# Performance work log

Measured on AMD Instinct MI355X. Metric: run time of the kernel, lower is better.

The kernel has to match this reference:

```python
import jax, jax.numpy as jnp
import numpy as np

D_MODEL = 1024
NUM_HEADS = 16
D_FF = 4096
EPS = 1e-5


def _linear(x, w, b):
    # torch nn.Linear: y = x @ W^T + b, W is [out, in]
    return jnp.einsum('bld,od->blo', x, w) + b


def _layer_norm(x, g, b):
    mu = jnp.mean(x, axis=-1, keepdims=True)
    var = jnp.mean(jnp.square(x - mu), axis=-1, keepdims=True)
    return (x - mu) / jnp.sqrt(var + EPS) * g + b


def _mha(q, k, v, wq, bq, wk, bk, wv, bv, wo, bo, mask, num_heads):
    B, Lq, D = q.shape
    hd = D // num_heads
    Q = _linear(q, wq, bq).reshape(B, Lq, num_heads, hd).transpose(0, 2, 1, 3)
    K = _linear(k, wk, bk).reshape(B, -1, num_heads, hd).transpose(0, 2, 1, 3)
    V = _linear(v, wv, bv).reshape(B, -1, num_heads, hd).transpose(0, 2, 1, 3)
    scale = jnp.sqrt(jnp.asarray(hd, dtype=q.dtype))
    energy = jnp.einsum('bhqd,bhkd->bhqk', Q, K) / scale  # [B,H,Lq,Lk]
    energy = jnp.where(mask, energy, jnp.asarray(-1e10, dtype=q.dtype))
    attn = jax.nn.softmax(energy, axis=-1)
    x = jnp.einsum('bhqk,bhkd->bhqd', attn, V)
    x = x.transpose(0, 2, 1, 3).reshape(B, Lq, D)
    return _linear(x, wo, bo), attn


def setup_inputs() -> dict:
    key = jax.random.key(0)
    ks = iter(jax.random.split(key, 40))
    B, T, S, D, F = 4, 1024, 1024, D_MODEL, D_FF
    inp = {
        'tgt': jax.random.normal(next(ks), (B, T, D), dtype=jnp.float32),
        'enc_src': jax.random.normal(next(ks), (B, S, D), dtype=jnp.float32),
        'tgt_mask': jnp.tril(jnp.ones((1, 1, T, T), dtype=bool)),
        'src_mask': jnp.ones((1, 1, 1, S), dtype=bool),
    }
    def lin(kk, o, i):
        return jax.random.normal(kk, (o, i), dtype=jnp.float32) * 0.02
    for pfx in ('sa', 'ca'):  # self-attn and cross-attn params
        for nm in ('q', 'k', 'v', 'o'):
            inp[f'{pfx}_w{nm}'] = lin(next(ks), D, D)
            inp[f'{pfx}_b{nm}'] = jnp.zeros((D,), dtype=jnp.float32)
    inp['ff_w1'] = lin(next(ks), F, D)
    inp['ff_b1'] = jnp.zeros((F,), dtype=jnp.float32)
    inp['ff_w2'] = lin(next(ks), D, F)
    inp['ff_b2'] = jnp.zeros((D,), dtype=jnp.float32)
    for i in (1, 2, 3):
        inp[f'ln{i}_g'] = jnp.ones((D,), dtype=jnp.float32)
        inp[f'ln{i}_b'] = jnp.zeros((D,), dtype=jnp.float32)
    return inp


def reference(tgt, enc_src, tgt_mask, src_mask,
              sa_wq, sa_bq, sa_wk, sa_bk, sa_wv, sa_bv, sa_wo, sa_bo,
              ca_wq, ca_bq, ca_wk, ca_bk, ca_wv, ca_bv, ca_wo, ca_bo,
              ff_w1, ff_b1, ff_w2, ff_b2,
              ln1_g, ln1_b, ln2_g, ln2_b, ln3_g, ln3_b):
    # dropout in eval mode (identity)
    _t, _ = _mha(tgt, tgt, tgt, sa_wq, sa_bq, sa_wk, sa_bk, sa_wv, sa_bv,
                 sa_wo, sa_bo, tgt_mask, NUM_HEADS)
    tgt = _layer_norm(tgt + _t, ln1_g, ln1_b)
    _t, attention = _mha(tgt, enc_src, enc_src, ca_wq, ca_bq, ca_wk, ca_bk,
                         ca_wv, ca_bv, ca_wo, ca_bo, src_mask, NUM_HEADS)
    tgt = _layer_norm(tgt + _t, ln2_g, ln2_b)
    _t = _linear(jax.nn.relu(_linear(tgt, ff_w1, ff_b1)), ff_w2, ff_b2)
    tgt = _layer_norm(tgt + _t, ln3_g, ln3_b)
    return tgt, attention
```

## Files before the change

### kernel.cpp

```cpp
#include <hip/hip_runtime.h>
#include <hip/hip_bf16.h>

#define BBATCH 4
#define TT 1024
#define SS 1024
#define DD 1024
#define HH 16
#define HD 64
#define FFD 4096
#define MM (BBATCH*TT)

using f32x4  = __attribute__((ext_vector_type(4))) float;
using s16x8  = __attribute__((ext_vector_type(8))) short;
using bf16x8 = __attribute__((ext_vector_type(8))) __bf16;

__device__ __forceinline__ unsigned short f2b(float f) {
  union { float f; unsigned int u; } x{f};
  unsigned int r = x.u + 0x7FFFu + ((x.u >> 16) & 1u);
  return (unsigned short)(r >> 16);
}

__device__ __forceinline__ float b2f(unsigned short u) {
  union { unsigned int i; float f; } x; x.i = (unsigned int)u << 16; return x.f;
}

__device__ __forceinline__ void gload16(const void* g, void* l) {
  __builtin_amdgcn_global_load_lds(
      (const __attribute__((address_space(1))) void*)g,
      (__attribute__((address_space(3))) void*)l, 16, 0, 0);
}

__device__ __forceinline__ f32x4 mfma_bf16(s16x8 a, s16x8 b, f32x4 c) {
  return __builtin_amdgcn_mfma_f32_16x16x32_bf16(
      __builtin_bit_cast(bf16x8, a), __builtin_bit_cast(bf16x8, b), c, 0, 0, 0);
}

template <int JT, int NSUB>
__device__ __forceinline__ void gemm_core(
    const unsigned short* __restrict__ Ab, int lda,
    const unsigned short* __restrict__ Bb, int ldb,
    int K, unsigned short* As, unsigned short* Bs, f32x4 (&acc)[4][JT])
{
  const int tid = threadIdx.x, wave = tid >> 6, lane = tid & 63;
  const int r0 = tid >> 2, c0 = (tid & 3) * 8;
  const int wrow = (wave >> 1) * 64, wcol = (wave & 1) * 16 * JT;
  const int q = lane >> 4, rl = lane & 15;
  const s16x8* Av = (const s16x8*)As;
  const s16x8* Bv = (const s16x8*)Bs;

  for (int k0 = 0; k0 < K; k0 += 32 * NSUB) {
#pragma unroll
    for (int s = 0; s < NSUB; s++) {
      int kk = k0 + s * 32;
      gload16(Ab + (size_t)r0 * lda + kk + c0, As + s * 4096 + wave * 512);
      gload16(Ab + (size_t)(r0 + 64) * lda + kk + c0, As + s * 4096 + wave * 512 + 2048);
      gload16(Bb + (size_t)r0 * ldb + kk + c0, Bs + s * (JT * 1024) + wave * 512);
      if (JT == 4)
        gload16(Bb + (size_t)(r0 + 64) * ldb + kk + c0, Bs + s * (JT * 1024) + wave * 512 + 2048);
    }
    __syncthreads();
#pragma unroll
    for (int s = 0; s < NSUB; s++) {
      s16x8 af[4], bfr[JT];
#pragma unroll
      for (int t = 0; t < 4; t++) af[t] = Av[s * 512 + (wrow + t * 16 + rl) * 4 + q];
#pragma unroll
      for (int t = 0; t < JT; t++) bfr[t] = Bv[s * (JT * 128) + (wcol + t * 16 + rl) * 4 + q];
#pragma unroll
      for (int i = 0; i < 4; i++)
#pragma unroll
        for (int j = 0; j < JT; j++)
          acc[i][j] = mfma_bf16(af[i], bfr[j], acc[i][j]);
    }
    __syncthreads();
  }
}

template <int EPI, int JT, int NSUB>
__global__ __launch_bounds__(256) void gemm_bt(
    const unsigned short* __restrict__ A, int lda,
    const unsigned short* __restrict__ B, int ldb,
    const float* __restrict__ bias, const float* __restrict__ res,
    float* __restrict__ Cf, unsigned short* __restrict__ Cb, int ldc, int K)
{
  __shared__ __align__(16) unsigned short As[NSUB * 128 * 32];
  __shared__ __align__(16) unsigned short Bs[NSUB * JT * 1024];
  const int bm = blockIdx.y, bn = blockIdx.x;
  const int lane = threadIdx.x & 63, wave = threadIdx.x >> 6;
  const int wrow = (wave >> 1) * 64, wcol = (wave & 1) * 16 * JT;
  const int q = lane >> 4, rl = lane & 15;

  f32x4 acc[4][JT];
  f32x4 z = {0.f, 0.f, 0.f, 0.f};
#pragma unroll
  for (int i = 0; i < 4; i++)
#pragma unroll
    for (int j = 0; j < JT; j++) acc[i][j] = z;

  gemm_core<JT, NSUB>(A + (size_t)bm * 128 * lda, lda,
                      B + (size_t)bn * (32 * JT) * ldb, ldb, K, As, Bs, acc);

#pragma unroll
  for (int i = 0; i < 4; i++) {
    int gm0 = bm * 128 + wrow + i * 16 + q * 4;
#pragma unroll
    for (int j = 0; j < JT; j++) {
      int gn = bn * (32 * JT) + wcol + j * 16 + rl;
      float bv = bias[gn];
#pragma unroll
      for (int r = 0; r < 4; r++) {
        size_t off = (size_t)(gm0 + r) * ldc + gn;
        float v = acc[i][j][r];
        if constexpr (EPI == 0) Cb[off] = f2b(v + bv);
        else if constexpr (EPI == 2) Cf[off] = v + bv + res[off];
        else Cb[off] = f2b(fmaxf(v + bv, 0.f));
      }
    }
  }
}

__device__ __forceinline__ void sblock_qk(
    const unsigned short* Qs, const unsigned short* Ks,
    int wrow, int wcol, int q, int rl, f32x4 (&acc)[4][4])
{
  const s16x8* Qv = (const s16x8*)Qs;
  const s16x8* Kv = (const s16x8*)Ks;
  f32x4 z = {0.f, 0.f, 0.f, 0.f};
#pragma unroll
  for (int i = 0; i < 4; i++)
#pragma unroll
    for (int j = 0; j < 4; j++) acc[i][j] = z;
#pragma unroll
  for (int kq = 0; kq < 2; kq++) {
    s16x8 af[4], bf[4];
#pragma unroll
    for (int t = 0; t < 4; t++) af[t] = Qv[kq * 512 + (wrow + t * 16 + rl) * 4 + q];
#pragma unroll
    for (int t = 0; t < 4; t++) bf[t] = Kv[kq * 512 + (wcol + t * 16 + rl) * 4 + q];
#pragma unroll
    for (int i = 0; i < 4; i++)
#pragma unroll
      for (int j = 0; j < 4; j++)
        acc[i][j] = mfma_bf16(af[i], bf[j], acc[i][j]);
  }
}

__device__ __forceinline__ void store_ps_swz(
    unsigned short* Ps, const f32x4 (&acc)[4][4], int wrow, int wcol, int q, int rl)
{
#pragma unroll
  for (int i = 0; i < 4; i++)
#pragma unroll
    for (int j = 0; j < 4; j++) {
      int col = wcol + j * 16 + rl;
      int ks = col >> 5, cc = col & 31;
#pragma unroll
      for (int r = 0; r < 4; r++) {
        int row = wrow + i * 16 + q * 4 + r;
        int unit = (row * 4 + (cc >> 3)) ^ ((row >> 1) & 3);
        Ps[ks * 4096 + unit * 8 + (cc & 7)] = f2b(acc[i][j][r]);
      }
    }
}

__device__ __forceinline__ void pv_swz(
    const unsigned short* Ps, const unsigned short* Vs,
    int wrow, int wc2, int q, int rl, f32x4 (&oacc)[4][2])
{
  const s16x8* Pv = (const s16x8*)Ps;
  const s16x8* Vv = (const s16x8*)Vs;
#pragma unroll
  for (int ks = 0; ks < 4; ks++) {
    s16x8 af[4], bf[2];
#pragma unroll
    for (int t = 0; t < 4; t++) {
      int row = wrow + t * 16 + rl;
      af[t] = Pv[ks * 512 + ((row * 4 + q) ^ ((row >> 1) & 3))];
    }
#pragma unroll
    for (int t = 0; t < 2; t++) bf[t] = Vv[ks * 256 + (wc2 + t * 16 + rl) * 4 + q];
#pragma unroll
    for (int i = 0; i < 4; i++)
#pragma unroll
      for (int jt = 0; jt < 2; jt++)
        oacc[i][jt] = mfma_bf16(af[i], bf[jt], oacc[i][jt]);
  }
}

__global__ __launch_bounds__(256, 2) void flash_sa(
    const unsigned short* __restrict__ Qg, int ldq,
    const unsigned short* __restrict__ Kg, int ldk,
    const unsigned short* __restrict__ Vt,
    unsigned short* __restrict__ Og)
{
  __shared__ __align__(16) unsigned short Qs[2 * 128 * 32];
  __shared__ __align__(16) unsigned short Ks[2 * 128 * 32];
  __shared__ __align__(16) unsigned short Vs[4 * 64 * 32];
  __shared__ __align__(16) unsigned short Ps[4 * 128 * 32];

  const int tid = threadIdx.x, wave = tid >> 6, lane = tid & 63;
  const int q = lane >> 4, rl = lane & 15;
  const int bh = blockIdx.y, b = bh >> 4, h = bh & 15;
  const int bm = (bh & 32) ? (7 - blockIdx.x) : blockIdx.x;
  const int wrow = (wave >> 1) * 64, wcol = (wave & 1) * 64;
  const int wc2 = (wave & 1) * 32;
  const int r0 = tid >> 2, c0 = (tid & 3) * 8;

  const unsigned short* Qbase = Qg + ((size_t)b * TT + bm * 128) * ldq + h * HD;
  const unsigned short* Kbase = Kg + (size_t)b * SS * ldk + h * HD;
  const unsigned short* Vbase = Vt + ((size_t)bh << 16);

#pragma unroll
  for (int kq = 0; kq < 2; kq++) {
    gload16(Qbase + (size_t)r0 * ldq + kq * 32 + c0, Qs + kq * 4096 + wave * 512);
    gload16(Qbase + (size_t)(r0 + 64) * ldq + kq * 32 + c0, Qs + kq * 4096 + wave * 512 + 2048);
  }
  const int nch = bm + 1;

  float l_run[4][4];
  f32x4 oacc[4][2];
  f32x4 z = {0.f, 0.f, 0.f, 0.f};
#pragma unroll
  for (int i = 0; i < 4; i++) {
    oacc[i][0] = z; oacc[i][1] = z;
#pragma unroll
    for (int r = 0; r < 4; r++) l_run[i][r] = 0.f;
  }

  for (int c = 0; c < nch; c++) {
    const unsigned short* src = Kbase + (size_t)c * 128 * ldk;
#pragma unroll
    for (int kq = 0; kq < 2; kq++) {
      gload16(src + (size_t)r0 * ldk + kq * 32 + c0, Ks + kq * 4096 + wave * 512);
      gload16(src + (size_t)(r0 + 64) * ldk + kq * 32 + c0, Ks + kq * 4096 + wave * 512 + 2048);
    }
#pragma unroll
    for (int ks = 0; ks < 4; ks++)
      gload16(Vbase + (size_t)r0 * SS + c * 128 + ks * 32 + c0, Vs + ks * 2048 + wave * 512);
    __syncthreads();

    f32x4 acc[4][4];
    sblock_qk(Qs, Ks, wrow, wcol, q, rl, acc);
#pragma unroll
    for (int i = 0; i < 4; i++)
#pragma unroll
      for (int r = 0; r < 4; r++) {
#pragma unroll
        for (int j = 0; j < 4; j++) {
          float v = acc[i][j][r] * 0.125f;
          bool msk = (c == bm) && (wcol + j * 16 + rl) > (wrow + i * 16 + q * 4 + r);
          acc[i][j][r] = msk ? 0.f : __expf(v);
        }
        float s = acc[i][0][r] + acc[i][1][r] + acc[i][2][r] + acc[i][3][r];
#pragma unroll
        for (int off = 1; off < 16; off <<= 1) s += __shfl_xor(s, off);
        l_run[i][r] += s;
      }
    store_ps_swz(Ps, acc, wrow, wcol, q, rl);
    __syncthreads();
    pv_swz(Ps, Vs, wrow, wc2, q, rl, oacc);
    __syncthreads();
  }

  float* red = (float*)Ps;
  if (rl == 0) {
#pragma unroll
    for (int i = 0; i < 4; i++)
#pragma unroll
      for (int r = 0; r < 4; r++)
        red[(wave & 1) * 128 + wrow + i * 16 + q * 4 + r] = l_run[i][r];
  }
  __syncthreads();

#pragma unroll
  for (int i = 0; i < 4; i++) {
#pragma unroll
    for (int r = 0; r < 4; r++) {
      int row = wrow + i * 16 + q * 4 + r;
      float inv = 1.0f / (red[row] + red[128 + row]);
      int grow = bm * 128 + row;
#pragma unroll
      for (int jt = 0; jt < 2; jt++) {
        int col = h * HD + wc2 + jt * 16 + rl;
        Og[((size_t)b * TT + grow) * DD + col] = f2b(oacc[i][jt][r] * inv);
      }
    }
  }
}

__global__ __launch_bounds__(256, 2) void flash_ca(
    const unsigned short* __restrict__ Qg, int ldq,
    const unsigned short* __restrict__ Kg, int ldk,
    const unsigned short* __restrict__ Vt,
    float* __restrict__ Pout,
    unsigned short* __restrict__ Og)
{
  __shared__ __align__(16) unsigned short Qs[2 * 128 * 32];
  __shared__ __align__(16) unsigned short Ks[2 * 128 * 32];
  __shared__ __align__(16) unsigned short Vs[4 * 64 * 32];
  __shared__ __align__(16) unsigned short Ps[4 * 128 * 32];

  const int tid = threadIdx.x, wave = tid >> 6, lane = tid & 63;
  const int q = lane >> 4, rl = lane & 15;
  const int bm = blockIdx.x, bh = blockIdx.y, b = bh >> 4, h = bh & 15;
  const int wrow = (wave >> 1) * 64, wcol = (wave & 1) * 64;
  const int wc2 = (wave & 1) * 32;
  const int r0 = tid >> 2, c0 = (tid & 3) * 8;

  const unsigned short* Qbase = Qg + ((size_t)b * TT + bm * 128) * ldq + h * HD;
  const unsigned short* Kbase = Kg + (size_t)b * SS * ldk + h * HD;
  const unsigned short* Vbase = Vt + ((size_t)bh << 16);

#pragma unroll
  for (int kq = 0; kq < 2; kq++) {
    gload16(Qbase + (size_t)r0 * ldq + kq * 32 + c0, Qs + kq * 4096 + wave * 512);
    gload16(Qbase + (size_t)(r0 + 64) * ldq + kq * 32 + c0, Qs + kq * 4096 + wave * 512 + 2048);
  }

  float l_run[4][4];
#pragma unroll
  for (int i = 0; i < 4; i++)
#pragma unroll
    for (int r = 0; r < 4; r++) l_run[i][r] = 0.f;

  for (int c = 0; c < 8; c++) {
    const unsigned short* src = Kbase + (size_t)c * 128 * ldk;
#pragma unroll
    for (int kq = 0; kq < 2; kq++) {
      gload16(src + (size_t)r0 * ldk + kq * 32 + c0, Ks + kq * 4096 + wave * 512);
      gload16(src + (size_t)(r0 + 64) * ldk + kq * 32 + c0, Ks + kq * 4096 + wave * 512 + 2048);
    }
    __syncthreads();
    f32x4 acc[4][4];
    sblock_qk(Qs, Ks, wrow, wcol, q, rl, acc);
#pragma unroll
    for (int i = 0; i < 4; i++)
#pragma unroll
      for (int r = 0; r < 4; r++) {
        float s = __expf(acc[i][0][r] * 0.125f) + __expf(acc[i][1][r] * 0.125f) +
                  __expf(acc[i][2][r] * 0.125f) + __expf(acc[i][3][r] * 0.125f);
#pragma unroll
        for (int off = 1; off < 16; off <<= 1) s += __shfl_xor(s, off);
        l_run[i][r] += s;
      }
    __syncthreads();
  }
  float* red = (float*)Ps;
  if (rl == 0) {
#pragma unroll
    for (int i = 0; i < 4; i++)
#pragma unroll
      for (int r = 0; r < 4; r++)
        red[(wave & 1) * 128 + wrow + i * 16 + q * 4 + r] = l_run[i][r];
  }
  __syncthreads();
  float invl[4][4];
#pragma unroll
  for (int i = 0; i < 4; i++)
#pragma unroll
    for (int r = 0; r < 4; r++) {
      int row = wrow + i * 16 + q * 4 + r;
      invl[i][r] = 1.0f / (red[row] + red[128 + row]);
    }

  f32x4 oacc[4][2];
  f32x4 z = {0.f, 0.f, 0.f, 0.f};
#pragma unroll
  for (int i = 0; i < 4; i++) { oacc[i][0] = z; oacc[i][1] = z; }

  for (int c = 0; c < 8; c++) {
    const unsigned short* src = Kbase + (size_t)c * 128 * ldk;
#pragma unroll
    for (int kq = 0; kq < 2; kq++) {
      gload16(src + (size_t)r0 * ldk + kq * 32 + c0, Ks + kq * 4096 + wave * 512);
      gload16(src + (size_t)(r0 + 64) * ldk + kq * 32 + c0, Ks + kq * 4096 + wave * 512 + 2048);
    }
#pragma unroll
    for (int ks = 0; ks < 4; ks++)
      gload16(Vbase + (size_t)r0 * SS + c * 128 + ks * 32 + c0, Vs + ks * 2048 + wave * 512);
    __syncthreads();
    f32x4 acc[4][4];
    sblock_qk(Qs, Ks, wrow, wcol, q, rl, acc);
#pragma unroll
    for (int i = 0; i < 4; i++)
#pragma unroll
      for (int j = 0; j < 4; j++)
#pragma unroll
        for (int r = 0; r < 4; r++)
          acc[i][j][r] = __expf(acc[i][j][r] * 0.125f) * invl[i][r];
    store_ps_swz(Ps, acc, wrow, wcol, q, rl);
    __syncthreads();
#pragma unroll
    for (int it = 0; it < 8; it++) {
      int idx = it * 256 + tid;
      int ks = idx >> 9, rw = (idx >> 2) & 127, u = idx & 3;
      s16x8 pv = ((const s16x8*)Ps)[ks * 512 + ((rw * 4 + u) ^ ((rw >> 1) & 3))];
      float4 lo = make_float4(b2f((unsigned short)pv[0]), b2f((unsigned short)pv[1]),
                              b2f((unsigned short)pv[2]), b2f((unsigned short)pv[3]));
      float4 hi = make_float4(b2f((unsigned short)pv[4]), b2f((unsigned short)pv[5]),
                              b2f((unsigned short)pv[6]), b2f((unsigned short)pv[7]));
      float* dst = Pout + ((size_t)bh << 20) + ((size_t)(bm * 128 + rw) << 10) +
                   c * 128 + ks * 32 + u * 8;
      ((float4*)dst)[0] = lo;
      ((float4*)dst)[1] = hi;
    }
    pv_swz(Ps, Vs, wrow, wc2, q, rl, oacc);
    __syncthreads();
  }

#pragma unroll
  for (int i = 0; i < 4; i++)
#pragma unroll
    for (int jt = 0; jt < 2; jt++)
#pragma unroll
      for (int r = 0; r < 4; r++) {
        int row = bm * 128 + wrow + i * 16 + q * 4 + r;
        int col = h * HD + wc2 + jt * 16 + rl;
        Og[((size_t)b * TT + row) * DD + col] = f2b(oacc[i][jt][r]);
      }
}

__global__ __launch_bounds__(256) void transpose_v(
    const unsigned short* __restrict__ V, int ldv, unsigned short* __restrict__ Vt)
{
  __shared__ unsigned short tile[64][68];
  const int bh = blockIdx.z, b = bh >> 4, h = bh & 15;
  const int s0 = blockIdx.x * 64;
  const int tid = threadIdx.x;
#pragma unroll
  for (int i = 0; i < 4; i++) {
    int idx = i * 256 + tid;
    int sl = idx >> 4, d0 = (idx & 15) * 4;
    ushort4 v = *(const ushort4*)&V[((size_t)b * SS + s0 + sl) * ldv + h * HD + d0];
    tile[sl][d0] = v.x; tile[sl][d0 + 1] = v.y; tile[sl][d0 + 2] = v.z; tile[sl][d0 + 3] = v.w;
  }
  __syncthreads();
#pragma unroll
  for (int i = 0; i < 4; i++) {
    int idx = i * 256 + tid;
    int d = idx >> 4, s4 = (idx & 15) * 4;
    ushort4 o = make_ushort4(tile[s4][d], tile[s4 + 1][d], tile[s4 + 2][d], tile[s4 + 3][d]);
    *(ushort4*)&Vt[((size_t)bh * HD + d) * SS + s0 + s4] = o;
  }
}

__global__ __launch_bounds__(256) void ln_k(
    const float* __restrict__ src, const float* __restrict__ g,
    const float* __restrict__ b, float* __restrict__ dstf,
    unsigned short* __restrict__ dstb)
{
  __shared__ float sh[10];
  const size_t row = blockIdx.x;
  const int tid = threadIdx.x;
  float4 v = ((const float4*)(src + (row << 10)))[tid];
  float s = v.x + v.y + v.z + v.w;
  float ss = v.x * v.x + v.y * v.y + v.z * v.z + v.w * v.w;
  for (int o = 32; o; o >>= 1) { s += __shfl_down(s, o); ss += __shfl_down(ss, o); }
  if ((tid & 63) == 0) { sh[tid >> 6] = s; sh[4 + (tid >> 6)] = ss; }
  __syncthreads();
  if (tid == 0) {
    sh[8] = sh[0] + sh[1] + sh[2] + sh[3];
    sh[9] = sh[4] + sh[5] + sh[6] + sh[7];
  }
  __syncthreads();
  const float mean = sh[8] * (1.0f / DD);
  const float var = sh[9] * (1.0f / DD) - mean * mean;
  const float inv = rsqrtf(var + 1e-5f);
  float4 gv = ((const float4*)g)[tid];
  float4 bv = ((const float4*)b)[tid];
  float4 y;
  y.x = (v.x - mean) * inv * gv.x + bv.x;
  y.y = (v.y - mean) * inv * gv.y + bv.y;
  y.z = (v.z - mean) * inv * gv.z + bv.z;
  y.w = (v.w - mean) * inv * gv.w + bv.w;
  if (dstf) ((float4*)(dstf + (row << 10)))[tid] = y;
  if (dstb) {
    ushort4 o = make_ushort4(f2b(y.x), f2b(y.y), f2b(y.z), f2b(y.w));
    ((ushort4*)(dstb + (row << 10)))[tid] = o;
  }
}

struct CvtArgs {
  const float* src[12];
  unsigned short* dst[12];
};

__global__ __launch_bounds__(256) void cvt_all(CvtArgs a) {
  constexpr int st[13] = {0,       1048576, 2097152, 2359296, 2621440,
                          2883584, 3145728, 3407872, 3670016, 3932160,
                          4194304, 5242880, 6291456};
  int i = blockIdx.x * 256 + threadIdx.x;
  int s = 0;
#pragma unroll
  for (int k = 1; k < 12; k++) s += (i >= st[k]) ? 1 : 0;
  int j = i - st[s];
  float4 v = ((const float4*)a.src[s])[j];
  ushort4 o = make_ushort4(f2b(v.x), f2b(v.y), f2b(v.z), f2b(v.w));
  ((ushort4*)a.dst[s])[j] = o;
}

__global__ __launch_bounds__(256) void bias_pack(
    const float* __restrict__ bq, const float* __restrict__ bk, const float* __restrict__ bv,
    const float* __restrict__ bk2, const float* __restrict__ bv2,
    float* __restrict__ bqkv, float* __restrict__ bkv)
{
  int i = blockIdx.x * 256 + threadIdx.x;
  if (i < 1024) bqkv[i] = bq[i];
  else if (i < 2048) bqkv[i] = bk[i - 1024];
  else if (i < 3072) bqkv[i] = bv[i - 2048];
  else if (i < 4096) bkv[i - 3072] = bk2[i - 3072];
  else if (i < 5120) bkv[i - 3072] = bv2[i - 4096 + 1024];
}


extern "C" void kernel_launch(void* const* d_in, const int* in_sizes, int n_in,
                              void* d_out, int out_size, void* d_ws, size_t ws_size,
                              hipStream_t stream)
{
  const float* tgt = (const float*)d_in[0];
  const float* enc = (const float*)d_in[1];
  const float* sa_wq = (const float*)d_in[4];  const float* sa_bq = (const float*)d_in[5];
  const float* sa_wk = (const float*)d_in[6];  const float* sa_bk = (const float*)d_in[7];
  const float* sa_wv = (const float*)d_in[8];  const float* sa_bv = (const float*)d_in[9];
  const float* sa_wo = (const float*)d_in[10]; const float* sa_bo = (const float*)d_in[11];
  const float* ca_wq = (const float*)d_in[12]; const float* ca_bq = (const float*)d_in[13];
  const float* ca_wk = (const float*)d_in[14]; const float* ca_bk = (const float*)d_in[15];
  const float* ca_wv = (const float*)d_in[16]; const float* ca_bv = (const float*)d_in[17];
  const float* ca_wo = (const float*)d_in[18]; const float* ca_bo = (const float*)d_in[19];
  const float* ff_w1 = (const float*)d_in[20]; const float* ff_b1 = (const float*)d_in[21];
  const float* ff_w2 = (const float*)d_in[22]; const float* ff_b2 = (const float*)d_in[23];
  const float* ln1_g = (const float*)d_in[24]; const float* ln1_b = (const float*)d_in[25];
  const float* ln2_g = (const float*)d_in[26]; const float* ln2_b = (const float*)d_in[27];
  const float* ln3_g = (const float*)d_in[28]; const float* ln3_b = (const float*)d_in[29];

  float* out_tgt = (float*)d_out;
  float* out_attn = (float*)d_out + (size_t)MM * DD;

  char* w = (char*)d_ws;
  size_t off = 0;
  auto alloc = [&](size_t bytes) { void* p = w + off; off += (bytes + 255) & ~(size_t)255; return p; };
  unsigned short* Xb   = (unsigned short*)alloc((size_t)MM * DD * 2);
  unsigned short* Eb   = (unsigned short*)alloc((size_t)MM * DD * 2);
  unsigned short* Wq1  = (unsigned short*)alloc((size_t)DD * DD * 2);
  unsigned short* Wk1  = (unsigned short*)alloc((size_t)DD * DD * 2);
  unsigned short* Wv1  = (unsigned short*)alloc((size_t)DD * DD * 2);
  unsigned short* Wo1  = (unsigned short*)alloc((size_t)DD * DD * 2);
  unsigned short* Wq2  = (unsigned short*)alloc((size_t)DD * DD * 2);
  unsigned short* Wk2  = (unsigned short*)alloc((size_t)DD * DD * 2);
  unsigned short* Wv2  = (unsigned short*)alloc((size_t)DD * DD * 2);
  unsigned short* Wo2  = (unsigned short*)alloc((size_t)DD * DD * 2);
  unsigned short* Wf1  = (unsigned short*)alloc((size_t)FFD * DD * 2);
  unsigned short* Wf2  = (unsigned short*)alloc((size_t)DD * FFD * 2);
  unsigned short* QKVb = (unsigned short*)alloc((size_t)MM * 3 * DD * 2);
  unsigned short* KVb  = (unsigned short*)alloc((size_t)MM * 2 * DD * 2);
  unsigned short* Qca  = (unsigned short*)alloc((size_t)MM * DD * 2);
  unsigned short* Vt   = (unsigned short*)alloc((size_t)MM * DD * 2);
  unsigned short* Ob   = (unsigned short*)alloc((size_t)MM * DD * 2);
  float*          res1 = (float*)alloc((size_t)MM * DD * 4);
  unsigned short* t1b  = (unsigned short*)alloc((size_t)MM * DD * 2);
  float*          res2 = (float*)alloc((size_t)MM * DD * 4);
  unsigned short* t2b  = (unsigned short*)alloc((size_t)MM * DD * 2);
  unsigned short* Fb   = (unsigned short*)alloc((size_t)MM * FFD * 2);
  float*          bqkv = (float*)alloc(3072 * 4);
  float*          bkv  = (float*)alloc(2048 * 4);

  CvtArgs ca;
  ca.src[0] = tgt;   ca.dst[0] = Xb;
  ca.src[1] = enc;   ca.dst[1] = Eb;
  ca.src[2] = sa_wq; ca.dst[2] = Wq1;
  ca.src[3] = sa_wk; ca.dst[3] = Wk1;
  ca.src[4] = sa_wv; ca.dst[4] = Wv1;
  ca.src[5] = sa_wo; ca.dst[5] = Wo1;
  ca.src[6] = ca_wq; ca.dst[6] = Wq2;
  ca.src[7] = ca_wk; ca.dst[7] = Wk2;
  ca.src[8] = ca_wv; ca.dst[8] = Wv2;
  ca.src[9] = ca_wo; ca.dst[9] = Wo2;
  ca.src[10] = ff_w1; ca.dst[10] = Wf1;
  ca.src[11] = ff_w2; ca.dst[11] = Wf2;

  bias_pack<<<20, 256, 0, stream>>>(sa_bq, sa_bk, sa_bv, ca_bk, ca_bv, bqkv, bkv);
  cvt_all<<<24576, 256, 0, stream>>>(ca);

  const dim3 gQKV(24, 32);
  const dim3 gKV(16, 32);
  const dim3 gN64(16, 32);
  const dim3 gFF1(32, 32);
  const dim3 gFl(8, 64);
  const dim3 gTr(SS / 64, 1, BBATCH * HH);

  gemm_bt<0, 4, 2><<<gQKV, 256, 0, stream>>>(Xb, DD, Wq1, DD, bqkv, nullptr, nullptr, QKVb, 3 * DD, DD);
  transpose_v<<<gTr, 256, 0, stream>>>(QKVb + 2 * DD, 3 * DD, Vt);
  flash_sa<<<gFl, 256, 0, stream>>>(QKVb, 3 * DD, QKVb + DD, 3 * DD, Vt, Ob);
  gemm_bt<2, 2, 4><<<gN64, 256, 0, stream>>>(Ob, DD, Wo1, DD, sa_bo, tgt, res1, nullptr, DD, DD);
  ln_k<<<MM, 256, 0, stream>>>(res1, ln1_g, ln1_b, res1, t1b);

  gemm_bt<0, 2, 4><<<gN64, 256, 0, stream>>>(t1b, DD, Wq2, DD, ca_bq, nullptr, nullptr, Qca, DD, DD);
  gemm_bt<0, 4, 2><<<gKV, 256, 0, stream>>>(Eb, DD, Wk2, DD, bkv, nullptr, nullptr, KVb, 2 * DD, DD);
  transpose_v<<<gTr, 256, 0, stream>>>(KVb + DD, 2 * DD, Vt);
  flash_ca<<<gFl, 256, 0, stream>>>(Qca, DD, KVb, 2 * DD, Vt, out_attn, Ob);
  gemm_bt<2, 2, 4><<<gN64, 256, 0, stream>>>(Ob, DD, Wo2, DD, ca_bo, res1, res2, nullptr, DD, DD);
  ln_k<<<MM, 256, 0, stream>>>(res2, ln2_g, ln2_b, res2, t2b);

  gemm_bt<3, 4, 2><<<gFF1, 256, 0, stream>>>(t2b, DD, Wf1, DD, ff_b1, nullptr, nullptr, Fb, FFD, DD);
  gemm_bt<2, 2, 4><<<gN64, 256, 0, stream>>>(Fb, FFD, Wf2, FFD, ff_b2, res2, res1, nullptr, DD, FFD);
  ln_k<<<MM, 256, 0, stream>>>(res1, ln3_g, ln3_b, out_tgt, nullptr);
}
```

Measured before the change: 786.7 us.

## Fuse self/cross QKV projections into one GEMM with transposed-V epilogue

Merges the self-attention QKV projection and the cross-attention KV projection (which depends only on encoder input) into a single 40x32-tile GEMM launch. Tiles that produce V write their output transposed through LDS directly into per-head Vt layout, which removes both transpose_v kernels. This saves two launches, a full read and write of V, and the tail effect of two separate GEMMs. In exchange it adds a second Vt buffer and some LDS reuse after the main loop. V columns are not written to QKVb/KVb, which is fine because the flash kernels read V from Vt.

```diff
diff --git a/kernel.cpp b/kernel.cpp
--- a/kernel.cpp
+++ b/kernel.cpp
@@ -115,6 +115,87 @@
         else if constexpr (EPI == 2) Cf[off] = v + bv + res[off];
         else Cb[off] = f2b(fmaxf(v + bv, 0.f));
       }
+    }
+  }
+}
+
+__global__ __launch_bounds__(256) void gemm_qkvkv(
+    const unsigned short* __restrict__ Xb, const unsigned short* __restrict__ Eb,
+    const unsigned short* __restrict__ Wqkv1, const unsigned short* __restrict__ Wkv2,
+    const float* __restrict__ bqkv, const float* __restrict__ bkv,
+    unsigned short* __restrict__ QKVb, unsigned short* __restrict__ KVb,
+    unsigned short* __restrict__ Vt1, unsigned short* __restrict__ Vt2)
+{
+  __shared__ __align__(16) unsigned short lds[16384];
+  unsigned short* As = lds;
+  unsigned short* Bs = lds + 8192;
+  const int tid = threadIdx.x;
+  const int bm = blockIdx.y, bn = blockIdx.x;
+  const int lane = tid & 63, wave = tid >> 6;
+  const int wrow = (wave >> 1) * 64, wcol = (wave & 1) * 64;
+  const int q = lane >> 4, rl = lane & 15;
+
+  const unsigned short *A, *Bw;
+  const float* bias;
+  unsigned short *C, *Vt;
+  int ldc, vbn;
+  bool isV;
+  if (bn < 24) {
+    A = Xb; Bw = Wqkv1 + (size_t)bn * 128 * 1024; bias = bqkv + bn * 128;
+    C = QKVb + bn * 128; ldc = 3072;
+    isV = (bn >= 16); Vt = Vt1; vbn = bn - 16;
+  } else {
+    int b2 = bn - 24;
+    A = Eb; Bw = Wkv2 + (size_t)b2 * 128 * 1024; bias = bkv + b2 * 128;
+    C = KVb + b2 * 128; ldc = 2048;
+    isV = (b2 >= 8); Vt = Vt2; vbn = b2 - 8;
+  }
+
+  f32x4 acc[4][4];
+  f32x4 z = {0.f, 0.f, 0.f, 0.f};
+#pragma unroll
+  for (int i = 0; i < 4; i++)
+#pragma unroll
+    for (int j = 0; j < 4; j++) acc[i][j] = z;
+
+  gemm_core<4, 2>(A + (size_t)bm * 128 * 1024, 1024, Bw, 1024, 1024, As, Bs, acc);
+
+  if (!isV) {
+#pragma unroll
+    for (int i = 0; i < 4; i++) {
+      int lr0 = wrow + i * 16 + q * 4;
+#pragma unroll
+      for (int j = 0; j < 4; j++) {
+        int lc = wcol + j * 16 + rl;
+        float bv = bias[lc];
+#pragma unroll
+        for (int r = 0; r < 4; r++)
+          C[(size_t)(bm * 128 + lr0 + r) * ldc + lc] = f2b(acc[i][j][r] + bv);
+      }
+    }
+  } else {
+#pragma unroll
+    for (int i = 0; i < 4; i++) {
+      int lr0 = wrow + i * 16 + q * 4;
+#pragma unroll
+      for (int j = 0; j < 4; j++) {
+        int lc = wcol + j * 16 + rl;
+        float bv = bias[lc];
+        int base = lc * 128, sw = (lc & 7) << 2;
+#pragma unroll
+        for (int r = 0; r < 4; r++)
+          lds[base + ((lr0 + r) ^ sw)] = f2b(acc[i][j][r] + bv);
+      }
+    }
+    __syncthreads();
+    const int b = bm >> 3, s0 = (bm & 7) * 128;
+#pragma unroll
+    for (int it = 0; it < 16; it++) {
+      int idx = it * 256 + tid;
+      int lc = idx >> 5, qa = idx & 31;
+      ushort4 v4 = *(const ushort4*)&lds[lc * 128 + ((qa ^ (lc & 7)) << 2)];
+      int h = vbn * 2 + (lc >> 6), d = lc & 63;
+      *(ushort4*)&Vt[(((size_t)b * 16 + h) * 64 + d) * 1024 + s0 + qa * 4] = v4;
     }
   }
 }
@@ -418,30 +499,6 @@
         int col = h * HD + wc2 + jt * 16 + rl;
         Og[((size_t)b * TT + row) * DD + col] = f2b(oacc[i][jt][r]);
       }
-}
-
-__global__ __launch_bounds__(256) void transpose_v(
-    const unsigned short* __restrict__ V, int ldv, unsigned short* __restrict__ Vt)
-{
-  __shared__ unsigned short tile[64][68];
-  const int bh = blockIdx.z, b = bh >> 4, h = bh & 15;
-  const int s0 = blockIdx.x * 64;
-  const int tid = threadIdx.x;
-#pragma unroll
-  for (int i = 0; i < 4; i++) {
-    int idx = i * 256 + tid;
-    int sl = idx >> 4, d0 = (idx & 15) * 4;
-    ushort4 v = *(const ushort4*)&V[((size_t)b * SS + s0 + sl) * ldv + h * HD + d0];
-    tile[sl][d0] = v.x; tile[sl][d0 + 1] = v.y; tile[sl][d0 + 2] = v.z; tile[sl][d0 + 3] = v.w;
-  }
-  __syncthreads();
-#pragma unroll
-  for (int i = 0; i < 4; i++) {
-    int idx = i * 256 + tid;
-    int d = idx >> 4, s4 = (idx & 15) * 4;
-    ushort4 o = make_ushort4(tile[s4][d], tile[s4 + 1][d], tile[s4 + 2][d], tile[s4 + 3][d]);
-    *(ushort4*)&Vt[((size_t)bh * HD + d) * SS + s0 + s4] = o;
-  }
 }
 
 __global__ __launch_bounds__(256) void ln_k(
@@ -554,7 +611,8 @@
   unsigned short* QKVb = (unsigned short*)alloc((size_t)MM * 3 * DD * 2);
   unsigned short* KVb  = (unsigned short*)alloc((size_t)MM * 2 * DD * 2);
   unsigned short* Qca  = (unsigned short*)alloc((size_t)MM * DD * 2);
-  unsigned short* Vt   = (unsigned short*)alloc((size_t)MM * DD * 2);
+  unsigned short* Vt1  = (unsigned short*)alloc((size_t)MM * DD * 2);
+  unsigned short* Vt2  = (unsigned short*)alloc((size_t)MM * DD * 2);
   unsigned short* Ob   = (unsigned short*)alloc((size_t)MM * DD * 2);
   float*          res1 = (float*)alloc((size_t)MM * DD * 4);
   unsigned short* t1b  = (unsigned short*)alloc((size_t)MM * DD * 2);
@@ -581,23 +639,20 @@
   bias_pack<<<20, 256, 0, stream>>>(sa_bq, sa_bk, sa_bv, ca_bk, ca_bv, bqkv, bkv);
   cvt_all<<<24576, 256, 0, stream>>>(ca);
 
-  const dim3 gQKV(24, 32);
-  const dim3 gKV(16, 32);
+  const dim3 gPRJ(40, 32);
   const dim3 gN64(16, 32);
   const dim3 gFF1(32, 32);
   const dim3 gFl(8, 64);
-  const dim3 gTr(SS / 64, 1, BBATCH * HH);
-
-  gemm_bt<0, 4, 2><<<gQKV, 256, 0, stream>>>(Xb, DD, Wq1, DD, bqkv, nullptr, nullptr, QKVb, 3 * DD, DD);
-  transpose_v<<<gTr, 256, 0, stream>>>(QKVb + 2 * DD, 3 * DD, Vt);
-  flash_sa<<<gFl, 256, 0, stream>>>(QKVb, 3 * DD, QKVb + DD, 3 * DD, Vt, Ob);
+
+  gemm_qkvkv<<<gPRJ, 256, 0, stream>>>(Xb, Eb, Wq1, Wk2, bqkv, bkv,
+                                       QKVb, KVb, Vt1, Vt2);
+
+  flash_sa<<<gFl, 256, 0, stream>>>(QKVb, 3 * DD, QKVb + DD, 3 * DD, Vt1, Ob);
   gemm_bt<2, 2, 4><<<gN64, 256, 0, stream>>>(Ob, DD, Wo1, DD, sa_bo, tgt, res1, nullptr, DD, DD);
   ln_k<<<MM, 256, 0, stream>>>(res1, ln1_g, ln1_b, res1, t1b);
 
   gemm_bt<0, 2, 4><<<gN64, 256, 0, stream>>>(t1b, DD, Wq2, DD, ca_bq, nullptr, nullptr, Qca, DD, DD);
-  gemm_bt<0, 4, 2><<<gKV, 256, 0, stream>>>(Eb, DD, Wk2, DD, bkv, nullptr, nullptr, KVb, 2 * DD, DD);
-  transpose_v<<<gTr, 256, 0, stream>>>(KVb + DD, 2 * DD, Vt);
-  flash_ca<<<gFl, 256, 0, stream>>>(Qca, DD, KVb, 2 * DD, Vt, out_attn, Ob);
+  flash_ca<<<gFl, 256, 0, stream>>>(Qca, DD, KVb, 2 * DD, Vt2, out_attn, Ob);
   gemm_bt<2, 2, 4><<<gN64, 256, 0, stream>>>(Ob, DD, Wo2, DD, ca_bo, res1, res2, nullptr, DD, DD);
   ln_k<<<MM, 256, 0, stream>>>(res2, ln2_g, ln2_b, res2, t2b);
 
```

New measurement: 781.4 us. Within noise of the previous version (-0.7%).
